# Kernel tuning notes

Measured on AMD Instinct MI355X. Metric: run time of the kernel, lower is better.

## Reference

```python
import jax, jax.numpy as jnp
import numpy as np

N = 50000      # nodes
E = 800000     # edges (before self loops)
IN = 256       # in_channels
HID = 64       # hidden_channels
HEADS = 2
NEG_SLOPE = 0.2
BN_EPS = 1e-5


def setup_inputs() -> dict:
    key = jax.random.key(0)
    ks = jax.random.split(key, 16)
    def g(i, shape, scale=0.05):
        return jax.random.normal(ks[i], shape, dtype=jnp.float32) * scale
    return {
        "x": jax.random.normal(ks[0], (N, IN), dtype=jnp.float32),
        "edge_index": jax.random.randint(ks[1], (2, E), 0, N, dtype=jnp.int64).astype(jnp.int32),
        # conv1 (GATv2, heads=2, concat)
        "W1l": g(2, (IN, HEADS * HID)), "b1l": jnp.zeros(HEADS * HID, jnp.float32),
        "W1r": g(3, (IN, HEADS * HID)), "b1r": jnp.zeros(HEADS * HID, jnp.float32),
        "att1": g(4, (HEADS, HID)), "bias1": jnp.zeros(HEADS * HID, jnp.float32),
        "bn1_g": jnp.ones(HEADS * HID, jnp.float32), "bn1_b": jnp.zeros(HEADS * HID, jnp.float32),
        "bn1_m": jnp.zeros(HEADS * HID, jnp.float32), "bn1_v": jnp.ones(HEADS * HID, jnp.float32),
        # conv2 (GATv2, heads=1)
        "W2l": g(5, (HEADS * HID, HID)), "b2l": jnp.zeros(HID, jnp.float32),
        "W2r": g(6, (HEADS * HID, HID)), "b2r": jnp.zeros(HID, jnp.float32),
        "att2": g(7, (1, HID)), "bias2": jnp.zeros(HID, jnp.float32),
        "bn2_g": jnp.ones(HID, jnp.float32), "bn2_b": jnp.zeros(HID, jnp.float32),
        "bn2_m": jnp.zeros(HID, jnp.float32), "bn2_v": jnp.ones(HID, jnp.float32),
        # classifier
        "Wc": g(8, (HID, 1)), "bc": jnp.zeros(1, jnp.float32),
    }


def _gatv2(x, src, dst, Wl, bl, Wr, br, att, bias, heads, ch, n):
    # GATv2: e_ij = att . leaky_relu(Wl x_j + Wr x_i); segment softmax over dst; out_i = sum alpha_ij Wl x_j
    xl = (x @ Wl + bl).reshape(n, heads, ch)  # source transform [N,H,C]
    xr = (x @ Wr + br).reshape(n, heads, ch)  # target transform [N,H,C]
    e = jax.nn.leaky_relu(xl[src] + xr[dst], NEG_SLOPE)        # [E,H,C]
    logits = jnp.einsum('ehc,hc->eh', e, att)                  # [E,H]
    m = jax.ops.segment_max(logits, dst, num_segments=n)       # [N,H]
    p = jnp.exp(logits - m[dst])
    s = jax.ops.segment_sum(p, dst, num_segments=n)            # [N,H]
    alpha = p / s[dst]                                         # [E,H]
    out = jax.ops.segment_sum(alpha[:, :, None] * xl[src], dst, num_segments=n)  # [N,H,C]
    return out.reshape(n, heads * ch) + bias


def _bn(x, g, b, m, v):
    return (x - m) * jax.lax.rsqrt(v + BN_EPS) * g + b


def reference(x, edge_index, W1l, b1l, W1r, b1r, att1, bias1,
              bn1_g, bn1_b, bn1_m, bn1_v,
              W2l, b2l, W2r, b2r, att2, bias2,
              bn2_g, bn2_b, bn2_m, bn2_v, Wc, bc):
    n = x.shape[0]
    loop = jnp.arange(n, dtype=edge_index.dtype)  # add_self_loops=True
    src = jnp.concatenate([edge_index[0], loop])
    dst = jnp.concatenate([edge_index[1], loop])
    h = _gatv2(x, src, dst, W1l, b1l, W1r, b1r, att1, bias1, HEADS, HID, n)
    h = jax.nn.elu(_bn(h, bn1_g, bn1_b, bn1_m, bn1_v))
    h = _gatv2(h, src, dst, W2l, b2l, W2r, b2r, att2, bias2, 1, HID, n)
    h = jax.nn.elu(_bn(h, bn2_g, bn2_b, bn2_m, bn2_v))
    return jax.nn.sigmoid(h @ Wc + bc)
```

## Files before the change

kernel.cpp:

```cpp
#include <hip/hip_runtime.h>
#include <hip/hip_bf16.h>
#include <cstddef>

#define NN 50000
#define EE 800000
#define TE 850000
#define INC 256
#define C1 128
#define C2 64
#define NCHUNK 49

#define NB_COUNT 3321
#define NB_CAST  12500
#define NB_P1    256
#define NB_P2    128
#define NB_K1    (NB_COUNT + NB_CAST + NB_P1 + NB_P2)
#define NB_GEMM1 782
#define NB_K2    (NB_GEMM1 + NB_COUNT)

#define LOG2E 1.44269504088896340736f

typedef unsigned short ushort_t;
typedef short bf16x8 __attribute__((ext_vector_type(8)));
typedef float f32x4 __attribute__((ext_vector_type(4)));

__device__ inline ushort_t bf16r(float f) {
    unsigned u = __float_as_uint(f);
    unsigned r = (u + 0x7fffu + ((u >> 16) & 1u)) >> 16;
    return (ushort_t)r;
}
#define LOF(u) (__uint_as_float((u) << 16))
#define HIF(u) (__uint_as_float((u) & 0xffff0000u))
#define ELU(t) ((t) > 0.f ? (t) : (__expf(t) - 1.f))


__global__ void k_scan1(const int* __restrict__ deg, int* __restrict__ incl,
                        int* __restrict__ totals) {
    __shared__ int lds[1024];
    int t = threadIdx.x;
    int i = blockIdx.x * 1024 + t;
    int v = (i < NN) ? deg[i] : 0;
    lds[t] = v;
    __syncthreads();
    for (int off = 1; off < 1024; off <<= 1) {
        int add = (t >= off) ? lds[t - off] : 0;
        __syncthreads();
        lds[t] += add;
        __syncthreads();
    }
    if (i < NN) incl[i] = lds[t];
    if (t == 1023) totals[blockIdx.x] = lds[t];
}

__global__ void k_scan3(const int* __restrict__ incl, const int* __restrict__ deg,
                        const int* __restrict__ totals, int* __restrict__ rowstart) {
    int i = blockIdx.x * blockDim.x + threadIdx.x;
    if (i == 0) rowstart[NN] = TE;
    if (i >= NN) return;
    int chunk = blockIdx.x >> 2;
    int coff = 0;
    for (int c = 0; c < chunk; c++) coff += totals[c];
    rowstart[i] = incl[i] - deg[i] + coff;
}


__global__ __launch_bounds__(256) void k_stage1(
    const int* __restrict__ ei, int* __restrict__ deg, int* __restrict__ rank,
    const float* __restrict__ x, ushort_t* __restrict__ xb,
    const float* __restrict__ W1l, const float* __restrict__ W1r,
    const float* __restrict__ b1l, const float* __restrict__ b1r,
    ushort_t* __restrict__ Wt1, float* __restrict__ biasf1,
    const float* __restrict__ W2l, const float* __restrict__ W2r,
    const float* __restrict__ b2l, const float* __restrict__ b2r,
    ushort_t* __restrict__ Wt2, float* __restrict__ biasf2) {
    int b = blockIdx.x;
    int tid = threadIdx.x;
    if (b < NB_COUNT) {
        int e = b * 256 + tid;
        if (e < TE) {
            int dst = (e < EE) ? ei[EE + e] : (e - EE);
            rank[e] = atomicAdd(&deg[dst], 1);
        }
    } else if (b < NB_COUNT + NB_CAST) {
        int i = (b - NB_COUNT) * 256 + tid;
        float4 a = ((const float4*)x)[i];
        ushort4 o;
        o.x = bf16r(a.x); o.y = bf16r(a.y); o.z = bf16r(a.z); o.w = bf16r(a.w);
        ((ushort4*)xb)[i] = o;
    } else if (b < NB_COUNT + NB_CAST + NB_P1) {
        int n = b - NB_COUNT - NB_CAST;
        int k = tid;
        const float* W = (n < 128) ? W1l : W1r;
        int c = (n < 128) ? n : n - 128;
        Wt1[(size_t)n * 256 + k] = bf16r(W[(size_t)k * 128 + c]);
        if (n == 0) biasf1[k] = (k < 128) ? b1l[k] : b1r[k - 128];
    } else {
        int n = b - NB_COUNT - NB_CAST - NB_P1;
        int k = tid;
        if (k < 128) {
            const float* W = (n < 64) ? W2l : W2r;
            int c = (n < 64) ? n : n - 64;
            Wt2[(size_t)n * 128 + k] = bf16r(W[(size_t)k * 64 + c]);
            if (n == 0) biasf2[k] = (k < 64) ? b2l[k] : b2r[k - 64];
        }
    }
}


template <int K, int NCOL>
__device__ inline void gemm_body(const ushort_t* __restrict__ A,
                                 const ushort_t* __restrict__ Bt,
                                 const float* __restrict__ bias,
                                 ushort_t* __restrict__ C, int M,
                                 int bm, int bn, ushort_t* As, ushort_t* Bs) {
    int tid = threadIdx.x;
    int w = tid >> 6, l = tid & 63;
    int wm = (w & 1) * 64, wn = (w >> 1) * 64;
    int lm = l & 15, half = l >> 4;

    f32x4 zero = {0.f, 0.f, 0.f, 0.f};
    f32x4 acc[4][4];
#pragma unroll
    for (int a = 0; a < 4; a++)
#pragma unroll
        for (int b = 0; b < 4; b++) acc[a][b] = zero;

    for (int k0 = 0; k0 < K; k0 += 32) {
#pragma unroll
        for (int q = 0; q < 2; q++) {
            int seg = q * 256 + tid;
            int m = seg >> 2;
            int ko = (seg & 3) * 8;
            *(float4*)&As[m * 40 + ko] = *(const float4*)&A[(size_t)(bm + m) * K + k0 + ko];
            *(float4*)&Bs[m * 40 + ko] = *(const float4*)&Bt[(size_t)(bn + m) * K + k0 + ko];
        }
        __syncthreads();
        bf16x8 af[4], bfr[4];
#pragma unroll
        for (int mi = 0; mi < 4; mi++)
            af[mi] = *(const bf16x8*)&As[(wm + mi * 16 + lm) * 40 + half * 8];
#pragma unroll
        for (int ni = 0; ni < 4; ni++)
            bfr[ni] = *(const bf16x8*)&Bs[(wn + ni * 16 + lm) * 40 + half * 8];
#pragma unroll
        for (int mi = 0; mi < 4; mi++)
#pragma unroll
            for (int ni = 0; ni < 4; ni++)
                acc[mi][ni] = __builtin_amdgcn_mfma_f32_16x16x32_bf16(
                    af[mi], bfr[ni], acc[mi][ni], 0, 0, 0);
        __syncthreads();
    }
#pragma unroll
    for (int ni = 0; ni < 4; ni++) {
        int col = bn + wn + ni * 16 + lm;
        float bv = bias[col];
#pragma unroll
        for (int mi = 0; mi < 4; mi++) {
            int rbase = bm + wm + mi * 16 + half * 4;
#pragma unroll
            for (int r = 0; r < 4; r++) {
                int row = rbase + r;
                if (row < M) C[(size_t)row * NCOL + col] = bf16r(acc[mi][ni][r] + bv);
            }
        }
    }
}


__global__ __launch_bounds__(256) void k_gemm1_scatter(
    const ushort_t* __restrict__ A, const ushort_t* __restrict__ Bt,
    const float* __restrict__ bias, ushort_t* __restrict__ C,
    const int* __restrict__ ei, const int* __restrict__ rank,
    const int* __restrict__ rowstart, int* __restrict__ ssrc) {
    __shared__ __align__(16) ushort_t As[128 * 40];
    __shared__ __align__(16) ushort_t Bs[128 * 40];
    int b = blockIdx.x;
    if (b < NB_GEMM1) {
        int bm = (b >> 1) * 128;
        int bn = (b & 1) * 128;
        gemm_body<256, 256>(A, Bt, bias, C, NN, bm, bn, As, Bs);
    } else {
        int e = (b - NB_GEMM1) * 256 + threadIdx.x;
        if (e < TE) {
            int s, d;
            if (e < EE) { s = ei[e]; d = ei[EE + e]; }
            else        { s = e - EE; d = s; }
            ssrc[rowstart[d] + rank[e]] = s;
        }
    }
}

__global__ __launch_bounds__(256) void k_gemm2(
    const ushort_t* __restrict__ A, const ushort_t* __restrict__ Bt,
    const float* __restrict__ bias, ushort_t* __restrict__ C) {
    __shared__ __align__(16) ushort_t As[128 * 40];
    __shared__ __align__(16) ushort_t Bs[128 * 40];
    int bm = blockIdx.x * 128;
    gemm_body<128, 128>(A, Bt, bias, C, NN, bm, 0, As, Bs);
}


__global__ __launch_bounds__(256) void k_fused1(
    const ushort_t* __restrict__ xlr, const int* __restrict__ rowstart,
    const int* __restrict__ ssrc, const float* __restrict__ att,
    const float* __restrict__ bias,
    const float* __restrict__ g, const float* __restrict__ b,
    const float* __restrict__ m, const float* __restrict__ v,
    ushort_t* __restrict__ out) {
    int lane = threadIdx.x & 63;
    int i = blockIdx.x * 4 + (threadIdx.x >> 6);
    if (i >= NN) return;
    int hw = lane >> 5;
    int c2 = lane & 31;
    uint2 xru = *(const uint2*)&xlr[(size_t)i * 256 + 128 + 4 * c2];
    float xr0 = LOF(xru.x), xr1 = HIF(xru.x), xr2 = LOF(xru.y), xr3 = HIF(xru.y);
    float4 at = *(const float4*)&att[4 * c2];
    float4 a6 = make_float4(at.x * (0.6f * LOG2E), at.y * (0.6f * LOG2E),
                            at.z * (0.6f * LOG2E), at.w * (0.6f * LOG2E));
    float4 a4 = make_float4(at.x * (0.4f * LOG2E), at.y * (0.4f * LOG2E),
                            at.z * (0.4f * LOG2E), at.w * (0.4f * LOG2E));
    int row = rowstart[i], end = rowstart[i + 1];
    float a0 = 0.f, a1 = 0.f, a2 = 0.f, a3 = 0.f, s = 0.f;
    int j = row;
    for (; j + 8 <= end; j += 8) {
        int src[4];
        uint2 u[4];
#pragma unroll
        for (int k = 0; k < 4; k++) src[k] = ssrc[j + 2 * k + hw];
#pragma unroll
        for (int k = 0; k < 4; k++)
            u[k] = *(const uint2*)&xlr[(size_t)src[k] * 256 + 4 * c2];
        float d[4], f0[4], f1[4], f2[4], f3[4];
#pragma unroll
        for (int k = 0; k < 4; k++) {
            f0[k] = LOF(u[k].x); f1[k] = HIF(u[k].x);
            f2[k] = LOF(u[k].y); f3[k] = HIF(u[k].y);
            float t0 = f0[k] + xr0, t1 = f1[k] + xr1;
            float t2 = f2[k] + xr2, t3 = f3[k] + xr3;
            float dd = fmaf(a6.x, t0, a4.x * fabsf(t0));
            dd = fmaf(a6.y, t1, fmaf(a4.y, fabsf(t1), dd));
            dd = fmaf(a6.z, t2, fmaf(a4.z, fabsf(t2), dd));
            dd = fmaf(a6.w, t3, fmaf(a4.w, fabsf(t3), dd));
            d[k] = dd;
        }
#pragma unroll
        for (int o = 1; o <= 8; o <<= 1) {
#pragma unroll
            for (int k = 0; k < 4; k++) d[k] += __shfl_xor(d[k], o, 64);
        }
#pragma unroll
        for (int k = 0; k < 4; k++) {
            float p = exp2f(d[k]);
            a0 += p * f0[k]; a1 += p * f1[k];
            a2 += p * f2[k]; a3 += p * f3[k];
            s += p;
        }
    }
    for (; j < end; j += 2) {
        int je = j + hw;
        bool valid = je < end;
        int src = valid ? ssrc[je] : i;
        uint2 uu = *(const uint2*)&xlr[(size_t)src * 256 + 4 * c2];
        float f0 = LOF(uu.x), f1 = HIF(uu.x), f2 = LOF(uu.y), f3 = HIF(uu.y);
        float t0 = f0 + xr0, t1 = f1 + xr1, t2 = f2 + xr2, t3 = f3 + xr3;
        float dd = fmaf(a6.x, t0, a4.x * fabsf(t0));
        dd = fmaf(a6.y, t1, fmaf(a4.y, fabsf(t1), dd));
        dd = fmaf(a6.z, t2, fmaf(a4.z, fabsf(t2), dd));
        dd = fmaf(a6.w, t3, fmaf(a4.w, fabsf(t3), dd));
        dd += __shfl_xor(dd, 1, 64);
        dd += __shfl_xor(dd, 2, 64);
        dd += __shfl_xor(dd, 4, 64);
        dd += __shfl_xor(dd, 8, 64);
        float p = valid ? exp2f(dd) : 0.f;
        a0 += p * f0; a1 += p * f1; a2 += p * f2; a3 += p * f3;
        s += p;
    }
    a0 += __shfl_xor(a0, 32, 64);
    a1 += __shfl_xor(a1, 32, 64);
    a2 += __shfl_xor(a2, 32, 64);
    a3 += __shfl_xor(a3, 32, 64);
    s  += __shfl_xor(s, 32, 64);
    if (hw == 0) {
        float inv = 1.f / s;
        float4 bb = *(const float4*)&bias[4 * c2];
        float4 mm = *(const float4*)&m[4 * c2];
        float4 vv = *(const float4*)&v[4 * c2];
        float4 gg = *(const float4*)&g[4 * c2];
        float4 b2 = *(const float4*)&b[4 * c2];
        float o0 = a0 * inv + bb.x, o1 = a1 * inv + bb.y;
        float o2 = a2 * inv + bb.z, o3 = a3 * inv + bb.w;
        o0 = (o0 - mm.x) * rsqrtf(vv.x + 1e-5f) * gg.x + b2.x;
        o1 = (o1 - mm.y) * rsqrtf(vv.y + 1e-5f) * gg.y + b2.y;
        o2 = (o2 - mm.z) * rsqrtf(vv.z + 1e-5f) * gg.z + b2.z;
        o3 = (o3 - mm.w) * rsqrtf(vv.w + 1e-5f) * gg.w + b2.w;
        o0 = ELU(o0); o1 = ELU(o1); o2 = ELU(o2); o3 = ELU(o3);
        uint2 wp;
        wp.x = (unsigned)bf16r(o0) | ((unsigned)bf16r(o1) << 16);
        wp.y = (unsigned)bf16r(o2) | ((unsigned)bf16r(o3) << 16);
        *(uint2*)&out[(size_t)i * C1 + 4 * c2] = wp;
    }
}

__global__ __launch_bounds__(256) void k_fused2(
    const ushort_t* __restrict__ xlr, const int* __restrict__ rowstart,
    const int* __restrict__ ssrc, const float* __restrict__ att,
    const float* __restrict__ bias,
    const float* __restrict__ g, const float* __restrict__ b,
    const float* __restrict__ m, const float* __restrict__ v,
    const float* __restrict__ Wc, const float* __restrict__ bc,
    float* __restrict__ out) {
    int lane = threadIdx.x & 63;
    int i = blockIdx.x * 4 + (threadIdx.x >> 6);
    if (i >= NN) return;
    int qw = lane >> 4;
    int c4 = lane & 15;
    uint2 xru = *(const uint2*)&xlr[(size_t)i * 128 + 64 + 4 * c4];
    float xr0 = LOF(xru.x), xr1 = HIF(xru.x), xr2 = LOF(xru.y), xr3 = HIF(xru.y);
    float4 at = *(const float4*)&att[4 * c4];
    float4 a6 = make_float4(at.x * (0.6f * LOG2E), at.y * (0.6f * LOG2E),
                            at.z * (0.6f * LOG2E), at.w * (0.6f * LOG2E));
    float4 a4 = make_float4(at.x * (0.4f * LOG2E), at.y * (0.4f * LOG2E),
                            at.z * (0.4f * LOG2E), at.w * (0.4f * LOG2E));
    int row = rowstart[i], end = rowstart[i + 1];
    float a0 = 0.f, a1 = 0.f, a2 = 0.f, a3 = 0.f, s = 0.f;
    int j = row;
    for (; j + 8 <= end; j += 8) {
        int src[2];
        uint2 u[2];
#pragma unroll
        for (int k = 0; k < 2; k++) src[k] = ssrc[j + 4 * k + qw];
#pragma unroll
        for (int k = 0; k < 2; k++)
            u[k] = *(const uint2*)&xlr[(size_t)src[k] * 128 + 4 * c4];
        float d[2], f0[2], f1[2], f2[2], f3[2];
#pragma unroll
        for (int k = 0; k < 2; k++) {
            f0[k] = LOF(u[k].x); f1[k] = HIF(u[k].x);
            f2[k] = LOF(u[k].y); f3[k] = HIF(u[k].y);
            float t0 = f0[k] + xr0, t1 = f1[k] + xr1;
            float t2 = f2[k] + xr2, t3 = f3[k] + xr3;
            float dd = fmaf(a6.x, t0, a4.x * fabsf(t0));
            dd = fmaf(a6.y, t1, fmaf(a4.y, fabsf(t1), dd));
            dd = fmaf(a6.z, t2, fmaf(a4.z, fabsf(t2), dd));
            dd = fmaf(a6.w, t3, fmaf(a4.w, fabsf(t3), dd));
            d[k] = dd;
        }
#pragma unroll
        for (int o = 1; o <= 8; o <<= 1) {
#pragma unroll
            for (int k = 0; k < 2; k++) d[k] += __shfl_xor(d[k], o, 64);
        }
#pragma unroll
        for (int k = 0; k < 2; k++) {
            float p = exp2f(d[k]);
            a0 += p * f0[k]; a1 += p * f1[k];
            a2 += p * f2[k]; a3 += p * f3[k];
            s += p;
        }
    }
    for (; j < end; j += 4) {
        int je = j + qw;
        bool valid = je < end;
        int src = valid ? ssrc[je] : i;
        uint2 uu = *(const uint2*)&xlr[(size_t)src * 128 + 4 * c4];
        float f0 = LOF(uu.x), f1 = HIF(uu.x), f2 = LOF(uu.y), f3 = HIF(uu.y);
        float t0 = f0 + xr0, t1 = f1 + xr1, t2 = f2 + xr2, t3 = f3 + xr3;
        float dd = fmaf(a6.x, t0, a4.x * fabsf(t0));
        dd = fmaf(a6.y, t1, fmaf(a4.y, fabsf(t1), dd));
        dd = fmaf(a6.z, t2, fmaf(a4.z, fabsf(t2), dd));
        dd = fmaf(a6.w, t3, fmaf(a4.w, fabsf(t3), dd));
        dd += __shfl_xor(dd, 1, 64);
        dd += __shfl_xor(dd, 2, 64);
        dd += __shfl_xor(dd, 4, 64);
        dd += __shfl_xor(dd, 8, 64);
        float p = valid ? exp2f(dd) : 0.f;
        a0 += p * f0; a1 += p * f1; a2 += p * f2; a3 += p * f3;
        s += p;
    }
#pragma unroll
    for (int o = 16; o <= 32; o <<= 1) {
        a0 += __shfl_xor(a0, o, 64);
        a1 += __shfl_xor(a1, o, 64);
        a2 += __shfl_xor(a2, o, 64);
        a3 += __shfl_xor(a3, o, 64);
        s  += __shfl_xor(s, o, 64);
    }
    float inv = 1.f / s;
    float4 bb = *(const float4*)&bias[4 * c4];
    float4 mm = *(const float4*)&m[4 * c4];
    float4 vv = *(const float4*)&v[4 * c4];
    float4 gg = *(const float4*)&g[4 * c4];
    float4 b2 = *(const float4*)&b[4 * c4];
    float o0 = a0 * inv + bb.x, o1 = a1 * inv + bb.y;
    float o2 = a2 * inv + bb.z, o3 = a3 * inv + bb.w;
    o0 = (o0 - mm.x) * rsqrtf(vv.x + 1e-5f) * gg.x + b2.x;
    o1 = (o1 - mm.y) * rsqrtf(vv.y + 1e-5f) * gg.y + b2.y;
    o2 = (o2 - mm.z) * rsqrtf(vv.z + 1e-5f) * gg.z + b2.z;
    o3 = (o3 - mm.w) * rsqrtf(vv.w + 1e-5f) * gg.w + b2.w;
    o0 = ELU(o0); o1 = ELU(o1); o2 = ELU(o2); o3 = ELU(o3);
    float4 wc = *(const float4*)&Wc[4 * c4];
    float z = o0 * wc.x + o1 * wc.y + o2 * wc.z + o3 * wc.w;
    z += __shfl_xor(z, 1, 64);
    z += __shfl_xor(z, 2, 64);
    z += __shfl_xor(z, 4, 64);
    z += __shfl_xor(z, 8, 64);
    if (lane == 0) out[i] = 1.f / (1.f + __expf(-(z + bc[0])));
}


extern "C" void kernel_launch(void* const* d_in, const int* in_sizes, int n_in,
                              void* d_out, int out_size, void* d_ws, size_t ws_size,
                              hipStream_t stream) {
    const float* x    = (const float*)d_in[0];
    const int*   ei   = (const int*)d_in[1];
    const float* W1l  = (const float*)d_in[2];
    const float* b1l  = (const float*)d_in[3];
    const float* W1r  = (const float*)d_in[4];
    const float* b1r  = (const float*)d_in[5];
    const float* att1 = (const float*)d_in[6];
    const float* bias1= (const float*)d_in[7];
    const float* bn1g = (const float*)d_in[8];
    const float* bn1b = (const float*)d_in[9];
    const float* bn1m = (const float*)d_in[10];
    const float* bn1v = (const float*)d_in[11];
    const float* W2l  = (const float*)d_in[12];
    const float* b2l  = (const float*)d_in[13];
    const float* W2r  = (const float*)d_in[14];
    const float* b2r  = (const float*)d_in[15];
    const float* att2 = (const float*)d_in[16];
    const float* bias2= (const float*)d_in[17];
    const float* bn2g = (const float*)d_in[18];
    const float* bn2b = (const float*)d_in[19];
    const float* bn2m = (const float*)d_in[20];
    const float* bn2v = (const float*)d_in[21];
    const float* Wc   = (const float*)d_in[22];
    const float* bc   = (const float*)d_in[23];
    float* out = (float*)d_out;

    char* ws = (char*)d_ws;
    size_t off = 0;
    auto alloc = [&](size_t bytes) {
        size_t o = off;
        off += (bytes + 255) & ~(size_t)255;
        return o;
    };
    ushort_t* xb    = (ushort_t*)(ws + alloc((size_t)(NN + 128) * 256 * 2));
    ushort_t* xlr1  = (ushort_t*)(ws + alloc((size_t)NN * 256 * 2));
    ushort_t* h1b   = (ushort_t*)(ws + alloc((size_t)(NN + 128) * 128 * 2));
    ushort_t* Wt1   = (ushort_t*)(ws + alloc((size_t)256 * 256 * 2));
    float*    biasf1= (float*)(ws + alloc(256 * 4));
    ushort_t* Wt2   = (ushort_t*)(ws + alloc((size_t)128 * 128 * 2));
    float*    biasf2= (float*)(ws + alloc(128 * 4));
    int* deg      = (int*)(ws + alloc((size_t)NN * 4));
    int* incl     = (int*)(ws + alloc((size_t)NN * 4));
    int* rowstart = (int*)(ws + alloc((size_t)(NN + 1) * 4));
    int* totals   = (int*)(ws + alloc(64 * 4));
    int* rank     = (int*)(ws + alloc((size_t)TE * 4));
    int* ssrc     = (int*)(ws + alloc((size_t)TE * 4));
    ushort_t* xlr2 = xlr1;

    hipMemsetAsync(deg, 0, (size_t)NN * 4, stream);

    k_stage1<<<NB_K1, 256, 0, stream>>>(ei, deg, rank, x, xb,
                                        W1l, W1r, b1l, b1r, Wt1, biasf1,
                                        W2l, W2r, b2l, b2r, Wt2, biasf2);

    k_scan1<<<NCHUNK, 1024, 0, stream>>>(deg, incl, totals);
    k_scan3<<<(NN + 255) / 256, 256, 0, stream>>>(incl, deg, totals, rowstart);

    k_gemm1_scatter<<<NB_K2, 256, 0, stream>>>(xb, Wt1, biasf1, xlr1,
                                               ei, rank, rowstart, ssrc);

    k_fused1<<<(NN + 3) / 4, 256, 0, stream>>>(xlr1, rowstart, ssrc, att1, bias1,
                                               bn1g, bn1b, bn1m, bn1v, h1b);

    k_gemm2<<<(NN + 127) / 128, 256, 0, stream>>>(h1b, Wt2, biasf2, xlr2);
    k_fused2<<<(NN + 3) / 4, 256, 0, stream>>>(xlr2, rowstart, ssrc, att2, bias2,
                                               bn2g, bn2b, bn2m, bn2v, Wc, bc, out);
}
```

Measured before the change: 297.3 us.

## Fuse fp32-to-bf16 cast into GEMM1 load and widen edge-aggregation vectors

The GEMM1 tile loader now reads fp32 x directly and converts it to bf16 in registers, so the separate cast pass and the bf16 copy of x are gone. A small prep kernel replaces the memset, zeroing degrees while transposing the weights. GEMM1 now runs alongside the degree counting, and the CSR scatter becomes its own kernel. Both aggregation kernels switch to 16-byte (8-channel) gathers per lane with more edges handled in parallel per wave, which cuts the shuffle-reduction steps. GEMM1 now reads twice the A bytes in fp32, and the scatter can no longer overlap with the GEMM.

Result: slower. 307.6 us (+3.5%).

```diff
diff --git a/kernel.cpp b/kernel.cpp
--- a/kernel.cpp
+++ b/kernel.cpp
@@ -11,12 +11,10 @@
 #define NCHUNK 49
 
 #define NB_COUNT 3321
-#define NB_CAST  12500
-#define NB_P1    256
-#define NB_P2    128
-#define NB_K1    (NB_COUNT + NB_CAST + NB_P1 + NB_P2)
 #define NB_GEMM1 782
-#define NB_K2    (NB_GEMM1 + NB_COUNT)
+#define NB_K1    (NB_GEMM1 + NB_COUNT)
+#define NB_Z     196
+#define NB_PREP0 (NB_Z + 256 + 128)
 
 #define LOG2E 1.44269504088896340736f
 
@@ -29,9 +27,19 @@
     unsigned r = (u + 0x7fffu + ((u >> 16) & 1u)) >> 16;
     return (ushort_t)r;
 }
+__device__ inline unsigned packbf2(float a, float b) {
+    return (unsigned)bf16r(a) | ((unsigned)bf16r(b) << 16);
+}
 #define LOF(u) (__uint_as_float((u) << 16))
 #define HIF(u) (__uint_as_float((u) & 0xffff0000u))
 #define ELU(t) ((t) > 0.f ? (t) : (__expf(t) - 1.f))
+
+__device__ inline void unpack8(const uint4& u, float f[8]) {
+    f[0] = LOF(u.x); f[1] = HIF(u.x);
+    f[2] = LOF(u.y); f[3] = HIF(u.y);
+    f[4] = LOF(u.z); f[5] = HIF(u.z);
+    f[6] = LOF(u.w); f[7] = HIF(u.w);
+}
 
 
 __global__ void k_scan1(const int* __restrict__ deg, int* __restrict__ incl,
@@ -64,38 +72,27 @@
 }
 
 
-__global__ __launch_bounds__(256) void k_stage1(
-    const int* __restrict__ ei, int* __restrict__ deg, int* __restrict__ rank,
-    const float* __restrict__ x, ushort_t* __restrict__ xb,
+__global__ __launch_bounds__(256) void k_prep0(
+    int* __restrict__ deg,
     const float* __restrict__ W1l, const float* __restrict__ W1r,
     const float* __restrict__ b1l, const float* __restrict__ b1r,
     ushort_t* __restrict__ Wt1, float* __restrict__ biasf1,
     const float* __restrict__ W2l, const float* __restrict__ W2r,
     const float* __restrict__ b2l, const float* __restrict__ b2r,
     ushort_t* __restrict__ Wt2, float* __restrict__ biasf2) {
-    int b = blockIdx.x;
-    int tid = threadIdx.x;
-    if (b < NB_COUNT) {
-        int e = b * 256 + tid;
-        if (e < TE) {
-            int dst = (e < EE) ? ei[EE + e] : (e - EE);
-            rank[e] = atomicAdd(&deg[dst], 1);
-        }
-    } else if (b < NB_COUNT + NB_CAST) {
-        int i = (b - NB_COUNT) * 256 + tid;
-        float4 a = ((const float4*)x)[i];
-        ushort4 o;
-        o.x = bf16r(a.x); o.y = bf16r(a.y); o.z = bf16r(a.z); o.w = bf16r(a.w);
-        ((ushort4*)xb)[i] = o;
-    } else if (b < NB_COUNT + NB_CAST + NB_P1) {
-        int n = b - NB_COUNT - NB_CAST;
+    int b = blockIdx.x, tid = threadIdx.x;
+    if (b < NB_Z) {
+        int i = b * 256 + tid;
+        if (i < NN) deg[i] = 0;
+    } else if (b < NB_Z + 256) {
+        int n = b - NB_Z;
         int k = tid;
         const float* W = (n < 128) ? W1l : W1r;
         int c = (n < 128) ? n : n - 128;
         Wt1[(size_t)n * 256 + k] = bf16r(W[(size_t)k * 128 + c]);
         if (n == 0) biasf1[k] = (k < 128) ? b1l[k] : b1r[k - 128];
     } else {
-        int n = b - NB_COUNT - NB_CAST - NB_P1;
+        int n = b - NB_Z - 256;
         int k = tid;
         if (k < 128) {
             const float* W = (n < 64) ? W2l : W2r;
@@ -107,8 +104,8 @@
 }
 
 
-template <int K, int NCOL>
-__device__ inline void gemm_body(const ushort_t* __restrict__ A,
+template <int K, int NCOL, bool AF32>
+__device__ inline void gemm_body(const void* __restrict__ Aptr,
                                  const ushort_t* __restrict__ Bt,
                                  const float* __restrict__ bias,
                                  ushort_t* __restrict__ C, int M,
@@ -129,10 +126,25 @@
 #pragma unroll
         for (int q = 0; q < 2; q++) {
             int seg = q * 256 + tid;
-            int m = seg >> 2;
+            int mrow = seg >> 2;
             int ko = (seg & 3) * 8;
-            *(float4*)&As[m * 40 + ko] = *(const float4*)&A[(size_t)(bm + m) * K + k0 + ko];
-            *(float4*)&Bs[m * 40 + ko] = *(const float4*)&Bt[(size_t)(bn + m) * K + k0 + ko];
+            if constexpr (AF32) {
+                const float* A = (const float*)Aptr;
+                int r = bm + mrow;
+                if (r > M - 1) r = M - 1;
+                const float* ap = &A[(size_t)r * K + k0 + ko];
+                float4 lo = *(const float4*)ap;
+                float4 hi = *(const float4*)(ap + 4);
+                uint4 pk;
+                pk.x = packbf2(lo.x, lo.y); pk.y = packbf2(lo.z, lo.w);
+                pk.z = packbf2(hi.x, hi.y); pk.w = packbf2(hi.z, hi.w);
+                *(uint4*)&As[mrow * 40 + ko] = pk;
+            } else {
+                const ushort_t* A = (const ushort_t*)Aptr;
+                *(float4*)&As[mrow * 40 + ko] =
+                    *(const float4*)&A[(size_t)(bm + mrow) * K + k0 + ko];
+            }
+            *(float4*)&Bs[mrow * 40 + ko] = *(const float4*)&Bt[(size_t)(bn + mrow) * K + k0 + ko];
         }
         __syncthreads();
         bf16x8 af[4], bfr[4];
@@ -167,26 +179,36 @@
 }
 
 
-__global__ __launch_bounds__(256) void k_gemm1_scatter(
-    const ushort_t* __restrict__ A, const ushort_t* __restrict__ Bt,
-    const float* __restrict__ bias, ushort_t* __restrict__ C,
-    const int* __restrict__ ei, const int* __restrict__ rank,
-    const int* __restrict__ rowstart, int* __restrict__ ssrc) {
-    __shared__ __align__(16) ushort_t As[128 * 40];
-    __shared__ __align__(16) ushort_t Bs[128 * 40];
+__global__ __launch_bounds__(256) void k_stage1(
+    const int* __restrict__ ei, int* __restrict__ deg, int* __restrict__ rank,
+    const float* __restrict__ x, const ushort_t* __restrict__ Wt1,
+    const float* __restrict__ biasf1, ushort_t* __restrict__ xlr1) {
     int b = blockIdx.x;
     if (b < NB_GEMM1) {
+        __shared__ __align__(16) ushort_t As[128 * 40];
+        __shared__ __align__(16) ushort_t Bs[128 * 40];
         int bm = (b >> 1) * 128;
         int bn = (b & 1) * 128;
-        gemm_body<256, 256>(A, Bt, bias, C, NN, bm, bn, As, Bs);
+        gemm_body<256, 256, true>(x, Wt1, biasf1, xlr1, NN, bm, bn, As, Bs);
     } else {
         int e = (b - NB_GEMM1) * 256 + threadIdx.x;
         if (e < TE) {
-            int s, d;
-            if (e < EE) { s = ei[e]; d = ei[EE + e]; }
-            else        { s = e - EE; d = s; }
-            ssrc[rowstart[d] + rank[e]] = s;
-        }
+            int dst = (e < EE) ? ei[EE + e] : (e - EE);
+            rank[e] = atomicAdd(&deg[dst], 1);
+        }
+    }
+}
+
+
+__global__ __launch_bounds__(256) void k_scatter(
+    const int* __restrict__ ei, const int* __restrict__ rank,
+    const int* __restrict__ rowstart, int* __restrict__ ssrc) {
+    int e = blockIdx.x * 256 + threadIdx.x;
+    if (e < TE) {
+        int s, d;
+        if (e < EE) { s = ei[e]; d = ei[EE + e]; }
+        else        { s = e - EE; d = s; }
+        ssrc[rowstart[d] + rank[e]] = s;
     }
 }
 
@@ -196,7 +218,7 @@
     __shared__ __align__(16) ushort_t As[128 * 40];
     __shared__ __align__(16) ushort_t Bs[128 * 40];
     int bm = blockIdx.x * 128;
-    gemm_body<128, 128>(A, Bt, bias, C, NN, bm, 0, As, Bs);
+    gemm_body<128, 128, false>(A, Bt, bias, C, NN, bm, 0, As, Bs);
 }
 
 
@@ -210,96 +232,105 @@
     int lane = threadIdx.x & 63;
     int i = blockIdx.x * 4 + (threadIdx.x >> 6);
     if (i >= NN) return;
-    int hw = lane >> 5;
-    int c2 = lane & 31;
-    uint2 xru = *(const uint2*)&xlr[(size_t)i * 256 + 128 + 4 * c2];
-    float xr0 = LOF(xru.x), xr1 = HIF(xru.x), xr2 = LOF(xru.y), xr3 = HIF(xru.y);
-    float4 at = *(const float4*)&att[4 * c2];
-    float4 a6 = make_float4(at.x * (0.6f * LOG2E), at.y * (0.6f * LOG2E),
-                            at.z * (0.6f * LOG2E), at.w * (0.6f * LOG2E));
-    float4 a4 = make_float4(at.x * (0.4f * LOG2E), at.y * (0.4f * LOG2E),
-                            at.z * (0.4f * LOG2E), at.w * (0.4f * LOG2E));
+    int slot = lane >> 4;
+    int c8 = lane & 15;
+    const char* xb = (const char*)xlr;
+    unsigned coff = (unsigned)c8 << 4;
+    float xr[8];
+    { uint4 u = *(const uint4*)(xb + (((unsigned)i << 9) + 256u + coff)); unpack8(u, xr); }
+    float a6[8], a4[8];
+    {
+        const float* ap = att + 8 * c8;
+#pragma unroll
+        for (int c = 0; c < 8; c++) {
+            float a = ap[c];
+            a6[c] = a * (0.6f * LOG2E);
+            a4[c] = a * (0.4f * LOG2E);
+        }
+    }
     int row = rowstart[i], end = rowstart[i + 1];
-    float a0 = 0.f, a1 = 0.f, a2 = 0.f, a3 = 0.f, s = 0.f;
+    float acc[8] = {0.f, 0.f, 0.f, 0.f, 0.f, 0.f, 0.f, 0.f};
+    float s = 0.f;
     int j = row;
-    for (; j + 8 <= end; j += 8) {
+    for (; j + 16 <= end; j += 16) {
         int src[4];
-        uint2 u[4];
-#pragma unroll
-        for (int k = 0; k < 4; k++) src[k] = ssrc[j + 2 * k + hw];
+        uint4 u[4];
+#pragma unroll
+        for (int k = 0; k < 4; k++) src[k] = ssrc[j + 4 * k + slot];
 #pragma unroll
         for (int k = 0; k < 4; k++)
-            u[k] = *(const uint2*)&xlr[(size_t)src[k] * 256 + 4 * c2];
-        float d[4], f0[4], f1[4], f2[4], f3[4];
+            u[k] = *(const uint4*)(xb + (((unsigned)src[k] << 9) + coff));
 #pragma unroll
         for (int k = 0; k < 4; k++) {
-            f0[k] = LOF(u[k].x); f1[k] = HIF(u[k].x);
-            f2[k] = LOF(u[k].y); f3[k] = HIF(u[k].y);
-            float t0 = f0[k] + xr0, t1 = f1[k] + xr1;
-            float t2 = f2[k] + xr2, t3 = f3[k] + xr3;
-            float dd = fmaf(a6.x, t0, a4.x * fabsf(t0));
-            dd = fmaf(a6.y, t1, fmaf(a4.y, fabsf(t1), dd));
-            dd = fmaf(a6.z, t2, fmaf(a4.z, fabsf(t2), dd));
-            dd = fmaf(a6.w, t3, fmaf(a4.w, fabsf(t3), dd));
-            d[k] = dd;
-        }
-#pragma unroll
-        for (int o = 1; o <= 8; o <<= 1) {
-#pragma unroll
-            for (int k = 0; k < 4; k++) d[k] += __shfl_xor(d[k], o, 64);
-        }
-#pragma unroll
-        for (int k = 0; k < 4; k++) {
-            float p = exp2f(d[k]);
-            a0 += p * f0[k]; a1 += p * f1[k];
-            a2 += p * f2[k]; a3 += p * f3[k];
+            float f[8];
+            unpack8(u[k], f);
+            float t0 = f[0] + xr[0];
+            float dd = fmaf(a6[0], t0, a4[0] * fabsf(t0));
+#pragma unroll
+            for (int c = 1; c < 8; c++) {
+                float t = f[c] + xr[c];
+                dd = fmaf(a6[c], t, fmaf(a4[c], fabsf(t), dd));
+            }
+            dd += __shfl_xor(dd, 1, 64);
+            dd += __shfl_xor(dd, 2, 64);
+            dd += __shfl_xor(dd, 4, 64);
+            float p = exp2f(dd);
             s += p;
-        }
-    }
-    for (; j < end; j += 2) {
-        int je = j + hw;
+#pragma unroll
+            for (int c = 0; c < 8; c++) acc[c] = fmaf(p, f[c], acc[c]);
+        }
+    }
+    for (; j < end; j += 4) {
+        int je = j + slot;
         bool valid = je < end;
         int src = valid ? ssrc[je] : i;
-        uint2 uu = *(const uint2*)&xlr[(size_t)src * 256 + 4 * c2];
-        float f0 = LOF(uu.x), f1 = HIF(uu.x), f2 = LOF(uu.y), f3 = HIF(uu.y);
-        float t0 = f0 + xr0, t1 = f1 + xr1, t2 = f2 + xr2, t3 = f3 + xr3;
-        float dd = fmaf(a6.x, t0, a4.x * fabsf(t0));
-        dd = fmaf(a6.y, t1, fmaf(a4.y, fabsf(t1), dd));
-        dd = fmaf(a6.z, t2, fmaf(a4.z, fabsf(t2), dd));
-        dd = fmaf(a6.w, t3, fmaf(a4.w, fabsf(t3), dd));
+        uint4 uu = *(const uint4*)(xb + (((unsigned)src << 9) + coff));
+        float f[8];
+        unpack8(uu, f);
+        float t0 = f[0] + xr[0];
+        float dd = fmaf(a6[0], t0, a4[0] * fabsf(t0));
+#pragma unroll
+        for (int c = 1; c < 8; c++) {
+            float t = f[c] + xr[c];
+            dd = fmaf(a6[c], t, fmaf(a4[c], fabsf(t), dd));
+        }
         dd += __shfl_xor(dd, 1, 64);
         dd += __shfl_xor(dd, 2, 64);
         dd += __shfl_xor(dd, 4, 64);
-        dd += __shfl_xor(dd, 8, 64);
         float p = valid ? exp2f(dd) : 0.f;
-        a0 += p * f0; a1 += p * f1; a2 += p * f2; a3 += p * f3;
         s += p;
-    }
-    a0 += __shfl_xor(a0, 32, 64);
-    a1 += __shfl_xor(a1, 32, 64);
-    a2 += __shfl_xor(a2, 32, 64);
-    a3 += __shfl_xor(a3, 32, 64);
-    s  += __shfl_xor(s, 32, 64);
-    if (hw == 0) {
+#pragma unroll
+        for (int c = 0; c < 8; c++) acc[c] = fmaf(p, f[c], acc[c]);
+    }
+#pragma unroll
+    for (int o = 16; o <= 32; o <<= 1) {
+#pragma unroll
+        for (int c = 0; c < 8; c++) acc[c] += __shfl_xor(acc[c], o, 64);
+        s += __shfl_xor(s, o, 64);
+    }
+    if (slot == 0) {
         float inv = 1.f / s;
-        float4 bb = *(const float4*)&bias[4 * c2];
-        float4 mm = *(const float4*)&m[4 * c2];
-        float4 vv = *(const float4*)&v[4 * c2];
-        float4 gg = *(const float4*)&g[4 * c2];
-        float4 b2 = *(const float4*)&b[4 * c2];
-        float o0 = a0 * inv + bb.x, o1 = a1 * inv + bb.y;
-        float o2 = a2 * inv + bb.z, o3 = a3 * inv + bb.w;
-        o0 = (o0 - mm.x) * rsqrtf(vv.x + 1e-5f) * gg.x + b2.x;
-        o1 = (o1 - mm.y) * rsqrtf(vv.y + 1e-5f) * gg.y + b2.y;
-        o2 = (o2 - mm.z) * rsqrtf(vv.z + 1e-5f) * gg.z + b2.z;
-        o3 = (o3 - mm.w) * rsqrtf(vv.w + 1e-5f) * gg.w + b2.w;
-        o0 = ELU(o0); o1 = ELU(o1); o2 = ELU(o2); o3 = ELU(o3);
-        uint2 wp;
-        wp.x = (unsigned)bf16r(o0) | ((unsigned)bf16r(o1) << 16);
-        wp.y = (unsigned)bf16r(o2) | ((unsigned)bf16r(o3) << 16);
-        *(uint2*)&out[(size_t)i * C1 + 4 * c2] = wp;
-    }
-}
+        const float* bp = bias + 8 * c8;
+        const float* mp = m + 8 * c8;
+        const float* vp = v + 8 * c8;
+        const float* gp = g + 8 * c8;
+        const float* b2p = b + 8 * c8;
+        unsigned ov[4];
+#pragma unroll
+        for (int c = 0; c < 8; c += 2) {
+            float o0 = acc[c] * inv + bp[c];
+            float o1 = acc[c + 1] * inv + bp[c + 1];
+            o0 = (o0 - mp[c]) * rsqrtf(vp[c] + 1e-5f) * gp[c] + b2p[c];
+            o1 = (o1 - mp[c + 1]) * rsqrtf(vp[c + 1] + 1e-5f) * gp[c + 1] + b2p[c + 1];
+            o0 = ELU(o0); o1 = ELU(o1);
+            ov[c >> 1] = (unsigned)bf16r(o0) | ((unsigned)bf16r(o1) << 16);
+        }
+        uint4 w4;
+        w4.x = ov[0]; w4.y = ov[1]; w4.z = ov[2]; w4.w = ov[3];
+        *(uint4*)((char*)out + (((unsigned)i << 8) + coff)) = w4;
+    }
+}
+
 
 __global__ __launch_bounds__(256) void k_fused2(
     const ushort_t* __restrict__ xlr, const int* __restrict__ rowstart,
@@ -312,98 +343,100 @@
     int lane = threadIdx.x & 63;
     int i = blockIdx.x * 4 + (threadIdx.x >> 6);
     if (i >= NN) return;
-    int qw = lane >> 4;
-    int c4 = lane & 15;
-    uint2 xru = *(const uint2*)&xlr[(size_t)i * 128 + 64 + 4 * c4];
-    float xr0 = LOF(xru.x), xr1 = HIF(xru.x), xr2 = LOF(xru.y), xr3 = HIF(xru.y);
-    float4 at = *(const float4*)&att[4 * c4];
-    float4 a6 = make_float4(at.x * (0.6f * LOG2E), at.y * (0.6f * LOG2E),
-                            at.z * (0.6f * LOG2E), at.w * (0.6f * LOG2E));
-    float4 a4 = make_float4(at.x * (0.4f * LOG2E), at.y * (0.4f * LOG2E),
-                            at.z * (0.4f * LOG2E), at.w * (0.4f * LOG2E));
+    int slot = lane >> 3;
+    int c8 = lane & 7;
+    const char* xb = (const char*)xlr;
+    unsigned coff = (unsigned)c8 << 4;
+    float xr[8];
+    { uint4 u = *(const uint4*)(xb + (((unsigned)i << 8) + 128u + coff)); unpack8(u, xr); }
+    float a6[8], a4[8];
+    {
+        const float* ap = att + 8 * c8;
+#pragma unroll
+        for (int c = 0; c < 8; c++) {
+            float a = ap[c];
+            a6[c] = a * (0.6f * LOG2E);
+            a4[c] = a * (0.4f * LOG2E);
+        }
+    }
     int row = rowstart[i], end = rowstart[i + 1];
-    float a0 = 0.f, a1 = 0.f, a2 = 0.f, a3 = 0.f, s = 0.f;
+    float acc[8] = {0.f, 0.f, 0.f, 0.f, 0.f, 0.f, 0.f, 0.f};
+    float s = 0.f;
     int j = row;
-    for (; j + 8 <= end; j += 8) {
+    for (; j + 16 <= end; j += 16) {
         int src[2];
-        uint2 u[2];
-#pragma unroll
-        for (int k = 0; k < 2; k++) src[k] = ssrc[j + 4 * k + qw];
+        uint4 u[2];
+#pragma unroll
+        for (int k = 0; k < 2; k++) src[k] = ssrc[j + 8 * k + slot];
 #pragma unroll
         for (int k = 0; k < 2; k++)
-            u[k] = *(const uint2*)&xlr[(size_t)src[k] * 128 + 4 * c4];
-        float d[2], f0[2], f1[2], f2[2], f3[2];
+            u[k] = *(const uint4*)(xb + (((unsigned)src[k] << 8) + coff));
 #pragma unroll
         for (int k = 0; k < 2; k++) {
-            f0[k] = LOF(u[k].x); f1[k] = HIF(u[k].x);
-            f2[k] = LOF(u[k].y); f3[k] = HIF(u[k].y);
-            float t0 = f0[k] + xr0, t1 = f1[k] + xr1;
-            float t2 = f2[k] + xr2, t3 = f3[k] + xr3;
-            float dd = fmaf(a6.x, t0, a4.x * fabsf(t0));
-            dd = fmaf(a6.y, t1, fmaf(a4.y, fabsf(t1), dd));
-            dd = fmaf(a6.z, t2, fmaf(a4.z, fabsf(t2), dd));
-            dd = fmaf(a6.w, t3, fmaf(a4.w, fabsf(t3), dd));
-            d[k] = dd;
-        }
-#pragma unroll
-        for (int o = 1; o <= 8; o <<= 1) {
-#pragma unroll
-            for (int k = 0; k < 2; k++) d[k] += __shfl_xor(d[k], o, 64);
-        }
-#pragma unroll
-        for (int k = 0; k < 2; k++) {
-            float p = exp2f(d[k]);
-            a0 += p * f0[k]; a1 += p * f1[k];
-            a2 += p * f2[k]; a3 += p * f3[k];
+            float f[8];
+            unpack8(u[k], f);
+            float t0 = f[0] + xr[0];
+            float dd = fmaf(a6[0], t0, a4[0] * fabsf(t0));
+#pragma unroll
+            for (int c = 1; c < 8; c++) {
+                float t = f[c] + xr[c];
+                dd = fmaf(a6[c], t, fmaf(a4[c], fabsf(t), dd));
+            }
+            dd += __shfl_xor(dd, 1, 64);
+            dd += __shfl_xor(dd, 2, 64);
+            dd += __shfl_xor(dd, 4, 64);
+            float p = exp2f(dd);
             s += p;
-        }
-    }
-    for (; j < end; j += 4) {
-        int je = j + qw;
+#pragma unroll
+            for (int c = 0; c < 8; c++) acc[c] = fmaf(p, f[c], acc[c]);
+        }
+    }
+    for (; j < end; j += 8) {
+        int je = j + slot;
         bool valid = je < end;
         int src = valid ? ssrc[je] : i;
-        uint2 uu = *(const uint2*)&xlr[(size_t)src * 128 + 4 * c4];
-        float f0 = LOF(uu.x), f1 = HIF(uu.x), f2 = LOF(uu.y), f3 = HIF(uu.y);
-        float t0 = f0 + xr0, t1 = f1 + xr1, t2 = f2 + xr2, t3 = f3 + xr3;
-        float dd = fmaf(a6.x, t0, a4.x * fabsf(t0));
-        dd = fmaf(a6.y, t1, fmaf(a4.y, fabsf(t1), dd));
-        dd = fmaf(a6.z, t2, fmaf(a4.z, fabsf(t2), dd));
-        dd = fmaf(a6.w, t3, fmaf(a4.w, fabsf(t3), dd));
+        uint4 uu = *(const uint4*)(xb + (((unsigned)src << 8) + coff));
+        float f[8];
+        unpack8(uu, f);
+        float t0 = f[0] + xr[0];
+        float dd = fmaf(a6[0], t0, a4[0] * fabsf(t0));
+#pragma unroll
+        for (int c = 1; c < 8; c++) {
+            float t = f[c] + xr[c];
+            dd = fmaf(a6[c], t, fmaf(a4[c], fabsf(t), dd));
+        }
         dd += __shfl_xor(dd, 1, 64);
         dd += __shfl_xor(dd, 2, 64);
         dd += __shfl_xor(dd, 4, 64);
-        dd += __shfl_xor(dd, 8, 64);
         float p = valid ? exp2f(dd) : 0.f;
-        a0 += p * f0; a1 += p * f1; a2 += p * f2; a3 += p * f3;
         s += p;
-    }
-#pragma unroll
-    for (int o = 16; o <= 32; o <<= 1) {
-        a0 += __shfl_xor(a0, o, 64);
-        a1 += __shfl_xor(a1, o, 64);
-        a2 += __shfl_xor(a2, o, 64);
-        a3 += __shfl_xor(a3, o, 64);
-        s  += __shfl_xor(s, o, 64);
+#pragma unroll
+        for (int c = 0; c < 8; c++) acc[c] = fmaf(p, f[c], acc[c]);
+    }
+#pragma unroll
+    for (int o = 8; o <= 32; o <<= 1) {
+#pragma unroll
+        for (int c = 0; c < 8; c++) acc[c] += __shfl_xor(acc[c], o, 64);
+        s += __shfl_xor(s, o, 64);
     }
     float inv = 1.f / s;
-    float4 bb = *(const float4*)&bias[4 * c4];
-    float4 mm = *(const float4*)&m[4 * c4];
-    float4 vv = *(const float4*)&v[4 * c4];
-    float4 gg = *(const float4*)&g[4 * c4];
-    float4 b2 = *(const float4*)&b[4 * c4];
-    float o0 = a0 * inv + bb.x, o1 = a1 * inv + bb.y;
-    float o2 = a2 * inv + bb.z, o3 = a3 * inv + bb.w;
-    o0 = (o0 - mm.x) * rsqrtf(vv.x + 1e-5f) * gg.x + b2.x;
-    o1 = (o1 - mm.y) * rsqrtf(vv.y + 1e-5f) * gg.y + b2.y;
-    o2 = (o2 - mm.z) * rsqrtf(vv.z + 1e-5f) * gg.z + b2.z;
-    o3 = (o3 - mm.w) * rsqrtf(vv.w + 1e-5f) * gg.w + b2.w;
-    o0 = ELU(o0); o1 = ELU(o1); o2 = ELU(o2); o3 = ELU(o3);
-    float4 wc = *(const float4*)&Wc[4 * c4];
-    float z = o0 * wc.x + o1 * wc.y + o2 * wc.z + o3 * wc.w;
+    const float* bp = bias + 8 * c8;
+    const float* mp = m + 8 * c8;
+    const float* vp = v + 8 * c8;
+    const float* gp = g + 8 * c8;
+    const float* b2p = b + 8 * c8;
+    const float* wp = Wc + 8 * c8;
+    float z = 0.f;
+#pragma unroll
+    for (int c = 0; c < 8; c++) {
+        float o0 = acc[c] * inv + bp[c];
+        o0 = (o0 - mp[c]) * rsqrtf(vp[c] + 1e-5f) * gp[c] + b2p[c];
+        o0 = ELU(o0);
+        z = fmaf(o0, wp[c], z);
+    }
     z += __shfl_xor(z, 1, 64);
     z += __shfl_xor(z, 2, 64);
     z += __shfl_xor(z, 4, 64);
-    z += __shfl_xor(z, 8, 64);
     if (lane == 0) out[i] = 1.f / (1.f + __expf(-(z + bc[0])));
 }
 
@@ -444,7 +477,6 @@
         off += (bytes + 255) & ~(size_t)255;
         return o;
     };
-    ushort_t* xb    = (ushort_t*)(ws + alloc((size_t)(NN + 128) * 256 * 2));
     ushort_t* xlr1  = (ushort_t*)(ws + alloc((size_t)NN * 256 * 2));
     ushort_t* h1b   = (ushort_t*)(ws + alloc((size_t)(NN + 128) * 128 * 2));
     ushort_t* Wt1   = (ushort_t*)(ws + alloc((size_t)256 * 256 * 2));
@@ -459,17 +491,15 @@
     int* ssrc     = (int*)(ws + alloc((size_t)TE * 4));
     ushort_t* xlr2 = xlr1;
 
-    hipMemsetAsync(deg, 0, (size_t)NN * 4, stream);
-
-    k_stage1<<<NB_K1, 256, 0, stream>>>(ei, deg, rank, x, xb,
-                                        W1l, W1r, b1l, b1r, Wt1, biasf1,
-                                        W2l, W2r, b2l, b2r, Wt2, biasf2);
+    k_prep0<<<NB_PREP0, 256, 0, stream>>>(deg, W1l, W1r, b1l, b1r, Wt1, biasf1,
+                                          W2l, W2r, b2l, b2r, Wt2, biasf2);
+
+    k_stage1<<<NB_K1, 256, 0, stream>>>(ei, deg, rank, x, Wt1, biasf1, xlr1);
 
     k_scan1<<<NCHUNK, 1024, 0, stream>>>(deg, incl, totals);
     k_scan3<<<(NN + 255) / 256, 256, 0, stream>>>(incl, deg, totals, rowstart);
 
-    k_gemm1_scatter<<<NB_K2, 256, 0, stream>>>(xb, Wt1, biasf1, xlr1,
-                                               ei, rank, rowstart, ssrc);
+    k_scatter<<<NB_COUNT, 256, 0, stream>>>(ei, rank, rowstart, ssrc);
 
     k_fused1<<<(NN + 3) / 4, 256, 0, stream>>>(xlr1, rowstart, ssrc, att1, bias1,
                                                bn1g, bn1b, bn1m, bn1v, h1b);
```
